# Kernel optimization log

Hardware: AMD Instinct MI355X
Metric: run time of the kernel (lower is better)

The kernel has to match this reference:

```python
import jax, jax.numpy as jnp
import numpy as np

I, J, K = 64, 8192, 128  # agents, batch, comm_channels


def setup_inputs() -> dict:
    key = jax.random.key(0)
    ks = jax.random.split(key, 7)
    s = 1.0 / np.sqrt(K)  # roughly torch Linear init scale
    return {
        "x": jax.random.normal(ks[0], (I, J, K), dtype=jnp.float32),
        "Wv": jax.random.normal(ks[1], (K, K), dtype=jnp.float32) * s,
        "bv": jax.random.normal(ks[2], (K,), dtype=jnp.float32) * s,
        "Wq": jax.random.normal(ks[3], (K, K), dtype=jnp.float32) * s,
        "bq": jax.random.normal(ks[4], (K,), dtype=jnp.float32) * s,
        "Wk": jax.random.normal(ks[5], (K, K), dtype=jnp.float32) * s,
        "bk": jax.random.normal(ks[6], (K,), dtype=jnp.float32) * s,
        "index": 3,
    }


def reference(x, Wv, bv, Wq, bq, Wk, bk, index):
    # x: [I, J, K] = torch.cat(input_comms, 0)
    v = jnp.einsum('ijk,ck->ijc', x, Wv) + bv          # [I, J, K]
    q = jnp.einsum('ijk,ck->ijc', x, Wq) + bq          # [I, J, K]
    k = jnp.einsum('jk,ck->jc', x[index], Wk) + bk     # [J, K] (gather one agent)
    att = jnp.einsum('ijk,jk->ij', q, k)               # [I, J]
    att = jax.nn.softmax(att, axis=0)                  # softmax over agents
    features = jnp.einsum('ij,ijk->jk', att, v)        # [J, K]
    return features
```

## Files before the change

kernel.cpp:

```cpp
#include <hip/hip_runtime.h>

#define NI 64
#define NJ 8192
#define NK 128
#define LOG2E 1.44269504088896340736f

typedef float f32x4 __attribute__((ext_vector_type(4)));

#define WS_M    0
#define WS_WVT  16384
#define WS_D    32768
#define WS_KQ   32896

__global__ __launch_bounds__(128) void precompute_kernel(
    const float* __restrict__ Wv, const float* __restrict__ Wq,
    const float* __restrict__ Wk, const float* __restrict__ bk,
    float* __restrict__ ws)
{
    const int b = blockIdx.x;
    const int k = threadIdx.x;
    float macc = 0.f, dacc = 0.f;
    for (int c = 0; c < NK; ++c) {
        float wq = Wq[c*NK + k];
        macc += Wk[c*NK + b] * wq;
        if (b == 0) dacc += bk[c] * wq;
    }
    ws[WS_M + b*NK + k] = macc;
    ws[WS_WVT + b*NK + k] = Wv[k*NK + b];
    if (b == 0) ws[WS_D + k] = dacc;
}

__global__ __launch_bounds__(256) void kq_kernel(
    const float* __restrict__ x, const int* __restrict__ pIdx,
    const float* __restrict__ ws, float* __restrict__ kqout)
{
    const int tid = threadIdx.x;
    const int k2  = tid & 63;
    const int wv  = tid >> 6;
    const int j0  = blockIdx.x * 16 + wv * 4;
    const int idx = *pIdx;
    const float* __restrict__ M  = ws + WS_M;
    const float* __restrict__ x3 = x + (size_t)idx * NJ * NK;

    const float* r0 = x3 + (size_t)(j0+0)*NK;
    const float* r1 = x3 + (size_t)(j0+1)*NK;
    const float* r2 = x3 + (size_t)(j0+2)*NK;
    const float* r3 = x3 + (size_t)(j0+3)*NK;

    float d0 = ws[WS_D + 2*k2], d1 = ws[WS_D + 2*k2 + 1];
    float2 acc[4];
#pragma unroll
    for (int jj = 0; jj < 4; ++jj) { acc[jj].x = d0; acc[jj].y = d1; }

#pragma unroll 2
    for (int kp = 0; kp < NK; kp += 4) {
        float4 x0 = *(const float4*)(r0 + kp);
        float4 x1 = *(const float4*)(r1 + kp);
        float4 x2 = *(const float4*)(r2 + kp);
        float4 x3v = *(const float4*)(r3 + kp);
        float2 m0 = *(const float2*)(M + (kp+0)*NK + 2*k2);
        float2 m1 = *(const float2*)(M + (kp+1)*NK + 2*k2);
        float2 m2 = *(const float2*)(M + (kp+2)*NK + 2*k2);
        float2 m3 = *(const float2*)(M + (kp+3)*NK + 2*k2);
        acc[0].x += x0.x*m0.x + x0.y*m1.x + x0.z*m2.x + x0.w*m3.x;
        acc[0].y += x0.x*m0.y + x0.y*m1.y + x0.z*m2.y + x0.w*m3.y;
        acc[1].x += x1.x*m0.x + x1.y*m1.x + x1.z*m2.x + x1.w*m3.x;
        acc[1].y += x1.x*m0.y + x1.y*m1.y + x1.z*m2.y + x1.w*m3.y;
        acc[2].x += x2.x*m0.x + x2.y*m1.x + x2.z*m2.x + x2.w*m3.x;
        acc[2].y += x2.x*m0.y + x2.y*m1.y + x2.z*m2.y + x2.w*m3.y;
        acc[3].x += x3v.x*m0.x + x3v.y*m1.x + x3v.z*m2.x + x3v.w*m3.x;
        acc[3].y += x3v.x*m0.y + x3v.y*m1.y + x3v.z*m2.y + x3v.w*m3.y;
    }
#pragma unroll
    for (int jj = 0; jj < 4; ++jj) {
        float2 o; o.x = acc[jj].x * LOG2E; o.y = acc[jj].y * LOG2E;
        *(float2*)(kqout + (size_t)(j0+jj)*NK + 2*k2) = o;
    }
}

__global__ __launch_bounds__(256, 4) void att_y_feat_kernel(
    const float* __restrict__ x, const float* __restrict__ ws,
    const float* __restrict__ bv, float* __restrict__ out)
{
    __shared__ float y_s[8][NK];

    const int tid  = threadIdx.x;
    const int lane = tid & 63;
    const int w    = tid >> 6;
    const int jj   = lane >> 5;
    const int lq   = lane & 31;
    const int k0   = lq * 4;
    const int j    = blockIdx.x * 8 + w * 2 + jj;
    const size_t ISTEP = (size_t)NJ * NK;

    const f32x4 kqv = *(const f32x4*)(ws + WS_KQ + (size_t)j * NK + k0);
    const float* xb = x + (size_t)j * NK + k0;

    float m = -3.0e38f, s = 0.f;
    f32x4 yacc = {0.f, 0.f, 0.f, 0.f};

    auto step = [&](f32x4 b) {
        float p = b[0]*kqv[0] + b[1]*kqv[1] + b[2]*kqv[2] + b[3]*kqv[3];
        p += __shfl_xor(p, 1);
        p += __shfl_xor(p, 2);
        p += __shfl_xor(p, 4);
        p += __shfl_xor(p, 8);
        p += __shfl_xor(p, 16);
        float mn = fmaxf(m, p);
        float sc = __builtin_amdgcn_exp2f(m - mn);
        float e  = __builtin_amdgcn_exp2f(p - mn);
        s = s * sc + e;
        yacc[0] = yacc[0]*sc + e*b[0];
        yacc[1] = yacc[1]*sc + e*b[1];
        yacc[2] = yacc[2]*sc + e*b[2];
        yacc[3] = yacc[3]*sc + e*b[3];
        m = mn;
    };

    f32x4 buf[8];
#pragma unroll
    for (int t = 0; t < 8; ++t)
        buf[t] = *(const f32x4*)(xb + (size_t)t * ISTEP);

    for (int ib = 0; ib < 7; ++ib) {
#pragma unroll
        for (int t = 0; t < 8; ++t) {
            f32x4 b = buf[t];
            buf[t] = *(const f32x4*)(xb + (size_t)((ib + 1) * 8 + t) * ISTEP);
            step(b);
        }
    }
#pragma unroll
    for (int t = 0; t < 8; ++t)
        step(buf[t]);

    float inv = 1.f / s;
    f32x4 yv = { yacc[0]*inv, yacc[1]*inv, yacc[2]*inv, yacc[3]*inv };
    *(f32x4*)&y_s[w*2 + jj][k0] = yv;
    __syncthreads();

    const int fj = tid >> 5;
    const int c0 = (tid & 31) * 4;
    const float* __restrict__ WvT = ws + WS_WVT;
    f32x4 acc = *(const f32x4*)(bv + c0);
#pragma unroll 8
    for (int kp = 0; kp < NK; ++kp) {
        float yk = y_s[fj][kp];
        f32x4 wv4 = *(const f32x4*)(WvT + (size_t)kp * NK + c0);
        acc[0] += yk * wv4[0]; acc[1] += yk * wv4[1];
        acc[2] += yk * wv4[2]; acc[3] += yk * wv4[3];
    }
    *(f32x4*)(out + (size_t)(blockIdx.x * 8 + fj) * NK + c0) = acc;
}

extern "C" void kernel_launch(void* const* d_in, const int* in_sizes, int n_in,
                              void* d_out, int out_size, void* d_ws, size_t ws_size,
                              hipStream_t stream) {
    const float* x  = (const float*)d_in[0];
    const float* Wv = (const float*)d_in[1];
    const float* bv = (const float*)d_in[2];
    const float* Wq = (const float*)d_in[3];
    const float* bq = (const float*)d_in[4];  (void)bq;
    const float* Wk = (const float*)d_in[5];
    const float* bk = (const float*)d_in[6];
    const int*  idx = (const int*)d_in[7];
    float* ws  = (float*)d_ws;
    float* out = (float*)d_out;

    precompute_kernel<<<NK, NK, 0, stream>>>(Wv, Wq, Wk, bk, ws);
    kq_kernel<<<NJ/16, 256, 0, stream>>>(x, idx, ws, ws + WS_KQ);
    att_y_feat_kernel<<<NJ/8, 256, 0, stream>>>(x, ws, bv, out);
}
```

Before: 99.45 us.

## Fuse kq projection into attention kernel and deepen x prefetch buffer

Removes the separate kq_kernel. Each attention block now loads its 8 rows of x[index] into shared memory and computes the kq vectors there, which drops one launch and the global round-trip of the kq intermediate. The per-thread prefetch buffer for the agent loop also grows from 8 to 16 float4 loads in flight. The cost is extra per-block prologue work with two more barriers, and higher register pressure under launch_bounds(256,4).

Measured after the change: 92.01 us. -7.5%, faster.

```diff
diff --git a/kernel.cpp b/kernel.cpp
--- a/kernel.cpp
+++ b/kernel.cpp
@@ -10,7 +10,6 @@
 #define WS_M    0
 #define WS_WVT  16384
 #define WS_D    32768
-#define WS_KQ   32896
 
 __global__ __launch_bounds__(128) void precompute_kernel(
     const float* __restrict__ Wv, const float* __restrict__ Wq,
@@ -30,58 +29,13 @@
     if (b == 0) ws[WS_D + k] = dacc;
 }
 
-__global__ __launch_bounds__(256) void kq_kernel(
-    const float* __restrict__ x, const int* __restrict__ pIdx,
-    const float* __restrict__ ws, float* __restrict__ kqout)
+__global__ __launch_bounds__(256, 4) void att_fused_kernel(
+    const float* __restrict__ x, const float* __restrict__ ws,
+    const float* __restrict__ bv, const int* __restrict__ pIdx,
+    float* __restrict__ out)
 {
-    const int tid = threadIdx.x;
-    const int k2  = tid & 63;
-    const int wv  = tid >> 6;
-    const int j0  = blockIdx.x * 16 + wv * 4;
-    const int idx = *pIdx;
-    const float* __restrict__ M  = ws + WS_M;
-    const float* __restrict__ x3 = x + (size_t)idx * NJ * NK;
-
-    const float* r0 = x3 + (size_t)(j0+0)*NK;
-    const float* r1 = x3 + (size_t)(j0+1)*NK;
-    const float* r2 = x3 + (size_t)(j0+2)*NK;
-    const float* r3 = x3 + (size_t)(j0+3)*NK;
-
-    float d0 = ws[WS_D + 2*k2], d1 = ws[WS_D + 2*k2 + 1];
-    float2 acc[4];
-#pragma unroll
-    for (int jj = 0; jj < 4; ++jj) { acc[jj].x = d0; acc[jj].y = d1; }
-
-#pragma unroll 2
-    for (int kp = 0; kp < NK; kp += 4) {
-        float4 x0 = *(const float4*)(r0 + kp);
-        float4 x1 = *(const float4*)(r1 + kp);
-        float4 x2 = *(const float4*)(r2 + kp);
-        float4 x3v = *(const float4*)(r3 + kp);
-        float2 m0 = *(const float2*)(M + (kp+0)*NK + 2*k2);
-        float2 m1 = *(const float2*)(M + (kp+1)*NK + 2*k2);
-        float2 m2 = *(const float2*)(M + (kp+2)*NK + 2*k2);
-        float2 m3 = *(const float2*)(M + (kp+3)*NK + 2*k2);
-        acc[0].x += x0.x*m0.x + x0.y*m1.x + x0.z*m2.x + x0.w*m3.x;
-        acc[0].y += x0.x*m0.y + x0.y*m1.y + x0.z*m2.y + x0.w*m3.y;
-        acc[1].x += x1.x*m0.x + x1.y*m1.x + x1.z*m2.x + x1.w*m3.x;
-        acc[1].y += x1.x*m0.y + x1.y*m1.y + x1.z*m2.y + x1.w*m3.y;
-        acc[2].x += x2.x*m0.x + x2.y*m1.x + x2.z*m2.x + x2.w*m3.x;
-        acc[2].y += x2.x*m0.y + x2.y*m1.y + x2.z*m2.y + x2.w*m3.y;
-        acc[3].x += x3v.x*m0.x + x3v.y*m1.x + x3v.z*m2.x + x3v.w*m3.x;
-        acc[3].y += x3v.x*m0.y + x3v.y*m1.y + x3v.z*m2.y + x3v.w*m3.y;
-    }
-#pragma unroll
-    for (int jj = 0; jj < 4; ++jj) {
-        float2 o; o.x = acc[jj].x * LOG2E; o.y = acc[jj].y * LOG2E;
-        *(float2*)(kqout + (size_t)(j0+jj)*NK + 2*k2) = o;
-    }
-}
-
-__global__ __launch_bounds__(256, 4) void att_y_feat_kernel(
-    const float* __restrict__ x, const float* __restrict__ ws,
-    const float* __restrict__ bv, float* __restrict__ out)
-{
+    __shared__ float x3_s[8][NK];
+    __shared__ float kq_s[8][NK];
     __shared__ float y_s[8][NK];
 
     const int tid  = threadIdx.x;
@@ -90,10 +44,37 @@
     const int jj   = lane >> 5;
     const int lq   = lane & 31;
     const int k0   = lq * 4;
-    const int j    = blockIdx.x * 8 + w * 2 + jj;
+    const int j0   = blockIdx.x * 8;
+    const int j    = j0 + w * 2 + jj;
     const size_t ISTEP = (size_t)NJ * NK;
+    const int idx  = *pIdx;
 
-    const f32x4 kqv = *(const f32x4*)(ws + WS_KQ + (size_t)j * NK + k0);
+    {
+        const float* src = x + (size_t)idx * ISTEP + (size_t)j0 * NK;
+        f32x4 v = *(const f32x4*)(src + 4 * tid);
+        const int r = (4 * tid) >> 7, c = (4 * tid) & 127;
+        *(f32x4*)&x3_s[r][c] = v;
+    }
+    __syncthreads();
+
+    {
+        const int r  = tid >> 5;
+        const int c0 = (tid & 31) * 4;
+        const float* __restrict__ M = ws + WS_M;
+        f32x4 acc = *(const f32x4*)(ws + WS_D + c0);
+#pragma unroll 8
+        for (int kp = 0; kp < NK; ++kp) {
+            float xv = x3_s[r][kp];
+            f32x4 mv = *(const f32x4*)(M + (size_t)kp * NK + c0);
+            acc[0] += xv * mv[0]; acc[1] += xv * mv[1];
+            acc[2] += xv * mv[2]; acc[3] += xv * mv[3];
+        }
+        acc[0] *= LOG2E; acc[1] *= LOG2E; acc[2] *= LOG2E; acc[3] *= LOG2E;
+        *(f32x4*)&kq_s[r][c0] = acc;
+    }
+    __syncthreads();
+
+    const f32x4 kqv = *(const f32x4*)&kq_s[w * 2 + jj][k0];
     const float* xb = x + (size_t)j * NK + k0;
 
     float m = -3.0e38f, s = 0.f;
@@ -117,40 +98,42 @@
         m = mn;
     };
 
-    f32x4 buf[8];
+    f32x4 buf[16];
 #pragma unroll
-    for (int t = 0; t < 8; ++t)
+    for (int t = 0; t < 16; ++t)
         buf[t] = *(const f32x4*)(xb + (size_t)t * ISTEP);
 
-    for (int ib = 0; ib < 7; ++ib) {
+    for (int ib = 0; ib < 3; ++ib) {
 #pragma unroll
-        for (int t = 0; t < 8; ++t) {
+        for (int t = 0; t < 16; ++t) {
             f32x4 b = buf[t];
-            buf[t] = *(const f32x4*)(xb + (size_t)((ib + 1) * 8 + t) * ISTEP);
+            buf[t] = *(const f32x4*)(xb + (size_t)((ib + 1) * 16 + t) * ISTEP);
             step(b);
         }
     }
 #pragma unroll
-    for (int t = 0; t < 8; ++t)
+    for (int t = 0; t < 16; ++t)
         step(buf[t]);
 
     float inv = 1.f / s;
-    f32x4 yv = { yacc[0]*inv, yacc[1]*inv, yacc[2]*inv, yacc[3]*inv };
-    *(f32x4*)&y_s[w*2 + jj][k0] = yv;
+    yacc[0] *= inv; yacc[1] *= inv; yacc[2] *= inv; yacc[3] *= inv;
+    *(f32x4*)&y_s[w * 2 + jj][k0] = yacc;
     __syncthreads();
 
-    const int fj = tid >> 5;
-    const int c0 = (tid & 31) * 4;
-    const float* __restrict__ WvT = ws + WS_WVT;
-    f32x4 acc = *(const f32x4*)(bv + c0);
+    {
+        const int fj = tid >> 5;
+        const int c0 = (tid & 31) * 4;
+        const float* __restrict__ WvT = ws + WS_WVT;
+        f32x4 acc = *(const f32x4*)(bv + c0);
 #pragma unroll 8
-    for (int kp = 0; kp < NK; ++kp) {
-        float yk = y_s[fj][kp];
-        f32x4 wv4 = *(const f32x4*)(WvT + (size_t)kp * NK + c0);
-        acc[0] += yk * wv4[0]; acc[1] += yk * wv4[1];
-        acc[2] += yk * wv4[2]; acc[3] += yk * wv4[3];
+        for (int kp = 0; kp < NK; ++kp) {
+            float yk = y_s[fj][kp];
+            f32x4 wv4 = *(const f32x4*)(WvT + (size_t)kp * NK + c0);
+            acc[0] += yk * wv4[0]; acc[1] += yk * wv4[1];
+            acc[2] += yk * wv4[2]; acc[3] += yk * wv4[3];
+        }
+        *(f32x4*)(out + (size_t)(j0 + fj) * NK + c0) = acc;
     }
-    *(f32x4*)(out + (size_t)(blockIdx.x * 8 + fj) * NK + c0) = acc;
 }
 
 extern "C" void kernel_launch(void* const* d_in, const int* in_sizes, int n_in,
@@ -168,6 +151,5 @@
     float* out = (float*)d_out;
 
     precompute_kernel<<<NK, NK, 0, stream>>>(Wv, Wq, Wk, bk, ws);
-    kq_kernel<<<NJ/16, 256, 0, stream>>>(x, idx, ws, ws + WS_KQ);
-    att_y_feat_kernel<<<NJ/8, 256, 0, stream>>>(x, ws, bv, out);
+    att_fused_kernel<<<NJ/8, 256, 0, stream>>>(x, ws, bv, idx, out);
 }
```
